# Optimization experiments

Measured on AMD Instinct MI355X. Metric: run time of the kernel, lower is better.

The kernel has to match this reference:

```python
import jax, jax.numpy as jnp
import numpy as np

N = 100_000      # nodes
E = 1_600_000    # edges (avg degree 16)
D_IN = 128
D_OUT = 128
K = 64           # low-rank attention rank


def setup_inputs() -> dict:
    key = jax.random.key(0)
    ks = jax.random.split(key, 6)
    s = lambda d: 1.0 / np.sqrt(d)
    return {
        "x": jax.random.normal(ks[0], (N, D_IN), dtype=jnp.float32),
        "edge_index": jax.random.randint(ks[1], (2, E), 0, N, dtype=jnp.int32),
        "W_gcn": jax.random.normal(ks[2], (D_IN, D_OUT), dtype=jnp.float32) * s(D_IN),
        "b_gcn": jnp.zeros((D_OUT,), jnp.float32),
        "W_att": jax.random.normal(ks[3], (D_IN, 4 * K), dtype=jnp.float32) * s(D_IN),
        "b_att": jnp.zeros((4 * K,), jnp.float32),
        "W_red": jax.random.normal(ks[4], (D_OUT + 2 * K, D_OUT), dtype=jnp.float32) * s(D_OUT + 2 * K),
        "b_red": jnp.zeros((D_OUT,), jnp.float32),
    }


def _forward(x, W_gcn, b_gcn, W_att, b_att, W_red, b_red, edge_index):
    n = x.shape[0]
    # --- GCN conv (symmetric normalization, self-loops), dropout = identity (eval) ---
    loop = jnp.arange(n, dtype=edge_index.dtype)
    src = jnp.concatenate([edge_index[0], loop])
    dst = jnp.concatenate([edge_index[1], loop])
    deg = jax.ops.segment_sum(jnp.ones_like(dst, dtype=x.dtype), dst, num_segments=n)
    dinv = jax.lax.rsqrt(deg)                      # deg >= 1 due to self-loops
    norm = dinv[src] * dinv[dst]                   # [E+n]
    h = x @ W_gcn                                  # [n, D_OUT]
    agg = jax.ops.segment_sum(h[src] * norm[:, None], dst, num_segments=n) + b_gcn
    x_local = jax.nn.relu(agg)

    # --- Low-rank global attention (LRGA) ---
    t = jax.nn.relu(x @ W_att + b_att)             # [n, 4K]
    U, V, Z, T = jnp.split(t, 4, axis=1)           # each [n, K]
    # joint_normalize2: scalar 1/mean(U @ (V^T @ 1_n))
    D = 1.0 / jnp.mean(U @ (V.T @ jnp.ones((n, 1), x.dtype)))
    res = (U @ (V.T @ Z)) * D                      # [n, K]
    x_global = jnp.concatenate([res, T], axis=1)   # [n, 2K]

    # --- fuse + dim reduce ---
    return jnp.concatenate([x_local, x_global], axis=1) @ W_red + b_red


def reference(x, edge_index, W_gcn, b_gcn, W_att, b_att, W_red, b_red):
    return _forward(x, W_gcn, b_gcn, W_att, b_att, W_red, b_red, edge_index)
```

## Files before the change

kernel.cpp:

```cpp
#include <hip/hip_runtime.h>

#define DIN   128
#define DOUT  128
#define KR    64
#define TCOLS 256
#define WCOLS 384
#define P_RED 1024
#define PSTR  4224

typedef unsigned short ushort_t;
typedef __attribute__((ext_vector_type(8))) short bf16x8;
typedef __attribute__((ext_vector_type(4))) float f32x4;

__device__ __forceinline__ float bf2f(unsigned short u) {
  return __uint_as_float(((unsigned int)u) << 16);
}
__device__ __forceinline__ unsigned short f2bf(float f) {
  unsigned int b = __float_as_uint(f);
  b = b + 0x7FFFu + ((b >> 16) & 1u);
  return (unsigned short)(b >> 16);
}

__global__ __launch_bounds__(256) void k_init(int* __restrict__ degc, float* __restrict__ VtZ,
                                              float* __restrict__ colsum, int N) {
  int i = blockIdx.x * 256 + threadIdx.x;
  if (i < N) degc[i] = 1;
  if (i < 4096) VtZ[i] = 0.f;
  if (i < 128) colsum[i] = 0.f;
}

__global__ __launch_bounds__(256) void k_deg(const int* __restrict__ ei, int* __restrict__ degc, int E) {
  int e = blockIdx.x * 256 + threadIdx.x;
  if (e < E) atomicAdd(&degc[ei[E + e]], 1);
}

__global__ __launch_bounds__(256) void k_split(const float* __restrict__ x,
                                               ushort_t* __restrict__ xh, ushort_t* __restrict__ xl4,
                                               int total4) {
  int i = blockIdx.x * 256 + threadIdx.x;
  int stride = gridDim.x * 256;
  for (; i < total4; i += stride) {
    float4 v = ((const float4*)x)[i];
    ushort4 h, l;
    h.x = f2bf(v.x); h.y = f2bf(v.y); h.z = f2bf(v.z); h.w = f2bf(v.w);
    l.x = f2bf(v.x - bf2f(h.x)); l.y = f2bf(v.y - bf2f(h.y));
    l.z = f2bf(v.z - bf2f(h.z)); l.w = f2bf(v.w - bf2f(h.w));
    ((ushort4*)xh)[i] = h;
    ((ushort4*)xl4)[i] = l;
  }
}

__global__ __launch_bounds__(128) void k_wprep(const float* __restrict__ Wg, const float* __restrict__ Wa,
                                               ushort_t* __restrict__ whT, ushort_t* __restrict__ wlT) {
  int n = blockIdx.x;
  int k = threadIdx.x;
  float v = (n < DOUT) ? Wg[(size_t)k * DOUT + n] : Wa[(size_t)k * TCOLS + (n - DOUT)];
  ushort_t h = f2bf(v);
  whT[(size_t)n * DIN + k] = h;
  wlT[(size_t)n * DIN + k] = f2bf(v - bf2f(h));
}

__global__ __launch_bounds__(256) void k_scan1(const int* __restrict__ degc, int* __restrict__ offs,
                                               int* __restrict__ bsums, int N) {
  __shared__ int s[256];
  int tid = threadIdx.x;
  int base = blockIdx.x * 1024 + tid * 4;
  int c[4], e[4];
#pragma unroll
  for (int q = 0; q < 4; ++q) c[q] = (base + q < N) ? (degc[base + q] - 1) : 0;
  e[0] = 0; e[1] = c[0]; e[2] = e[1] + c[1]; e[3] = e[2] + c[2];
  int tsum = e[3] + c[3];
  s[tid] = tsum; __syncthreads();
  for (int off = 1; off < 256; off <<= 1) {
    int v = (tid >= off) ? s[tid - off] : 0;
    __syncthreads();
    s[tid] += v;
    __syncthreads();
  }
  int tb = s[tid] - tsum;
#pragma unroll
  for (int q = 0; q < 4; ++q) if (base + q < N) offs[base + q] = tb + e[q];
  if (tid == 255) bsums[blockIdx.x] = s[255];
}

__global__ __launch_bounds__(128) void k_scan2(const int* __restrict__ bsums, int* __restrict__ boff,
                                               int* __restrict__ offs, int NBLK, int N) {
  __shared__ int s[128];
  int tid = threadIdx.x;
  int v = (tid < NBLK) ? bsums[tid] : 0;
  s[tid] = v; __syncthreads();
  for (int off = 1; off < 128; off <<= 1) {
    int u = (tid >= off) ? s[tid - off] : 0;
    __syncthreads();
    s[tid] += u;
    __syncthreads();
  }
  boff[tid] = s[tid] - v;
  if (tid == 127) offs[N] = s[127];
}

__global__ __launch_bounds__(256) void k_scan3(int* __restrict__ offs, const int* __restrict__ boff,
                                               const int* __restrict__ degc, float* __restrict__ dinv,
                                               int* __restrict__ cursor, int N) {
  int i = blockIdx.x * 256 + threadIdx.x;
  if (i < N) {
    offs[i] += boff[i >> 10];
    dinv[i] = rsqrtf((float)degc[i]);
    cursor[i] = 0;
  }
}

__global__ __launch_bounds__(256) void k_scatter(const int* __restrict__ ei, const int* __restrict__ offs,
                                                 int* __restrict__ cursor, const float* __restrict__ dinv,
                                                 int2* __restrict__ csr, int E) {
  int e = blockIdx.x * 256 + threadIdx.x;
  if (e < E) {
    int s = ei[e];
    int d = ei[E + e];
    int pos = atomicAdd(&cursor[d], 1);
    int2 q;
    q.x = s;
    q.y = __float_as_int(dinv[s] * dinv[d]);
    csr[offs[d] + pos] = q;
  }
}

#define LOADK(S, AH, AL, BH, BL)                                              \
  {                                                                           \
    int k0_ = (S) * 32 + lk;                                                  \
    _Pragma("unroll") for (int m_ = 0; m_ < 4; ++m_) {                        \
      AH[m_] = *(const bf16x8*)&xh[(size_t)rows[m_] * DIN + k0_];             \
      AL[m_] = *(const bf16x8*)&xlo[(size_t)rows[m_] * DIN + k0_];            \
    }                                                                         \
    _Pragma("unroll") for (int n_ = 0; n_ < 4; ++n_) {                        \
      int gc_ = gcb + n_ * 16 + lr;                                           \
      BH[n_] = *(const bf16x8*)&whT[(size_t)gc_ * DIN + k0_];                 \
      BL[n_] = *(const bf16x8*)&wlT[(size_t)gc_ * DIN + k0_];                 \
    }                                                                         \
  }

__global__ __launch_bounds__(256, 2) void k_gemm1_mfma(const ushort_t* __restrict__ xh,
                                                       const ushort_t* __restrict__ xlo,
                                                       const ushort_t* __restrict__ whT,
                                                       const ushort_t* __restrict__ wlT,
                                                       const float* __restrict__ ba,
                                                       ushort_t* __restrict__ hs, ushort_t* __restrict__ t,
                                                       int N) {
  int tid = threadIdx.x;
  int lane = tid & 63;
  int wave = tid >> 6;
  int wr = wave >> 1, wc = wave & 1;
  int colblk = blockIdx.x;
  int rowbase = blockIdx.y * 128 + wr * 64;
  int gcb = colblk * 128 + wc * 64;
  int lr = lane & 15;
  int lk = (lane >> 4) * 8;
  int rq = (lane >> 4) * 4;

  int rows[4];
#pragma unroll
  for (int m = 0; m < 4; ++m) {
    int r = rowbase + m * 16 + lr;
    rows[m] = (r < N) ? r : (N - 1);
  }

  f32x4 acc[4][4] = {};
  bf16x8 ah[2][4], al[2][4], bh[2][4], bl[2][4];

  LOADK(0, ah[0], al[0], bh[0], bl[0]);
#pragma unroll
  for (int s = 0; s < 4; ++s) {
    int cur = s & 1, nxt = cur ^ 1;
    if (s < 3) LOADK(s + 1, ah[nxt], al[nxt], bh[nxt], bl[nxt]);
#pragma unroll
    for (int m = 0; m < 4; ++m)
#pragma unroll
      for (int n = 0; n < 4; ++n) {
        acc[m][n] = __builtin_amdgcn_mfma_f32_16x16x32_bf16(ah[cur][m], bl[cur][n], acc[m][n], 0, 0, 0);
        acc[m][n] = __builtin_amdgcn_mfma_f32_16x16x32_bf16(al[cur][m], bh[cur][n], acc[m][n], 0, 0, 0);
        acc[m][n] = __builtin_amdgcn_mfma_f32_16x16x32_bf16(ah[cur][m], bh[cur][n], acc[m][n], 0, 0, 0);
      }
  }

  if (colblk == 0) {
#pragma unroll
    for (int m = 0; m < 4; ++m)
#pragma unroll
      for (int i = 0; i < 4; ++i) {
        int row = rowbase + m * 16 + rq + i;
        if (row < N) {
#pragma unroll
          for (int n = 0; n < 4; ++n)
            hs[(size_t)row * DOUT + gcb + n * 16 + lr] = f2bf(acc[m][n][i]);
        }
      }
  } else {
    float bav[4];
#pragma unroll
    for (int n = 0; n < 4; ++n) bav[n] = ba[gcb - DOUT + n * 16 + lr];
#pragma unroll
    for (int m = 0; m < 4; ++m)
#pragma unroll
      for (int i = 0; i < 4; ++i) {
        int row = rowbase + m * 16 + rq + i;
        if (row < N) {
#pragma unroll
          for (int n = 0; n < 4; ++n)
            t[(size_t)row * TCOLS + gcb - DOUT + n * 16 + lr] =
                f2bf(fmaxf(acc[m][n][i] + bav[n], 0.f));
        }
      }
  }
}

__global__ __launch_bounds__(256) void k_red(const ushort_t* __restrict__ t, float* __restrict__ part,
                                             int N) {
  __shared__ float csh[512];
  int tid = threadIdx.x;
  int lane = tid & 63;
  int w = tid >> 6;
  int lr = lane & 15;
  int lk = (lane >> 4) * 8;
  int vcol = 64 + w * 16 + lr;
  int col2 = lane * 2;

  f32x4 acc[4] = {};
  float cs0 = 0.f, cs1 = 0.f;
  int ntiles = (N + 31) >> 5;

  for (int tile = blockIdx.x; tile < ntiles; tile += gridDim.x) {
    int r0 = tile * 32;
    const ushort_t* base = &t[(size_t)r0 * TCOLS];
    bf16x8 a, b[4];
    if (r0 + 32 <= N) {
#pragma unroll
      for (int j = 0; j < 8; ++j)
        ((short*)&a)[j] = (short)base[(size_t)(lk + j) * TCOLS + vcol];
#pragma unroll
      for (int n = 0; n < 4; ++n)
#pragma unroll
        for (int j = 0; j < 8; ++j)
          ((short*)&b[n])[j] = (short)base[(size_t)(lk + j) * TCOLS + 128 + n * 16 + lr];
#pragma unroll
      for (int j = 0; j < 8; ++j) {
        ushort2 u = *(const ushort2*)&base[(size_t)(w * 8 + j) * TCOLS + col2];
        cs0 += bf2f(u.x); cs1 += bf2f(u.y);
      }
    } else {
#pragma unroll
      for (int j = 0; j < 8; ++j) {
        int r = r0 + lk + j;
        ((short*)&a)[j] = (r < N) ? (short)t[(size_t)r * TCOLS + vcol] : (short)0;
      }
#pragma unroll
      for (int n = 0; n < 4; ++n)
#pragma unroll
        for (int j = 0; j < 8; ++j) {
          int r = r0 + lk + j;
          ((short*)&b[n])[j] = (r < N) ? (short)t[(size_t)r * TCOLS + 128 + n * 16 + lr] : (short)0;
        }
#pragma unroll
      for (int j = 0; j < 8; ++j) {
        int r = r0 + w * 8 + j;
        if (r < N) {
          ushort2 u = *(const ushort2*)&t[(size_t)r * TCOLS + col2];
          cs0 += bf2f(u.x); cs1 += bf2f(u.y);
        }
      }
    }
#pragma unroll
    for (int n = 0; n < 4; ++n)
      acc[n] = __builtin_amdgcn_mfma_f32_16x16x32_bf16(a, b[n], acc[n], 0, 0, 0);
  }

  float* pb = &part[(size_t)blockIdx.x * PSTR];
  int rq = (lane >> 4) * 4;
#pragma unroll
  for (int n = 0; n < 4; ++n)
#pragma unroll
    for (int i = 0; i < 4; ++i)
      pb[(w * 16 + rq + i) * 64 + n * 16 + lr] = acc[n][i];

  csh[tid] = cs0;
  csh[256 + tid] = cs1;
  __syncthreads();
  if (w == 0) {
    float t0 = csh[lane] + csh[64 + lane] + csh[128 + lane] + csh[192 + lane];
    float t1 = csh[256 + lane] + csh[320 + lane] + csh[384 + lane] + csh[448 + lane];
    pb[4096 + col2] = t0;
    pb[4096 + col2 + 1] = t1;
  }
}

__global__ __launch_bounds__(256) void k_redsum(const float* __restrict__ part,
                                                float* __restrict__ VtZ, float* __restrict__ colsum) {
  __shared__ float s[256];
  int tid = threadIdx.x;
  int j = blockIdx.x * 64 + (tid & 63);
  int bc = tid >> 6;
  float a = 0.f;
#pragma unroll 4
  for (int b = bc; b < P_RED; b += 4) a += part[(size_t)b * PSTR + j];
  s[tid] = a;
  __syncthreads();
  if (bc == 0) {
    float v = s[tid] + s[tid + 64] + s[tid + 128] + s[tid + 192];
    if (j < 4096) VtZ[j] = v;
    else colsum[j - 4096] = v;
  }
}

__global__ __launch_bounds__(64) void k_d(const float* __restrict__ colsum, float* __restrict__ Dws, int N) {
  __shared__ float s[64];
  int k = threadIdx.x;
  s[k] = colsum[k] * colsum[64 + k];
  __syncthreads();
  for (int off = 32; off > 0; off >>= 1) {
    if (k < off) s[k] += s[k + off];
    __syncthreads();
  }
  if (k == 0) {
    float p = s[0];
    Dws[0] = (p != 0.f) ? ((float)N / p) : 0.f;
  }
}

__global__ __launch_bounds__(256) void k_prep(const float* __restrict__ VtZ,
                                              const float* __restrict__ Dws,
                                              const float* __restrict__ Wr,
                                              ushort_t* __restrict__ weffT) {
  int c = blockIdx.x;
  int k = threadIdx.x;
  float v;
  if (k < 128 || k >= 192) {
    v = Wr[(size_t)k * DOUT + c];
  } else {
    float Dv = Dws[0];
    int kk = k - 128;
    float acc = 0.f;
#pragma unroll 8
    for (int j = 0; j < 64; ++j)
      acc += VtZ[kk * 64 + j] * Wr[(size_t)(128 + j) * DOUT + c];
    v = acc * Dv;
  }
  weffT[(size_t)c * 256 + k] = f2bf(v);
}

__global__ __launch_bounds__(256) void k_out_mfma(const ushort_t* __restrict__ xl,
                                                  const ushort_t* __restrict__ t,
                                                  const ushort_t* __restrict__ weffT,
                                                  const float* __restrict__ br,
                                                  float* __restrict__ out, int N) {
  int tid = threadIdx.x;
  int lane = tid & 63;
  int wave = tid >> 6;
  int wr = wave >> 1, wc = wave & 1;
  int rowbase = blockIdx.x * 128 + wr * 64;
  int cbase = wc * 64;
  int lr = lane & 15;
  int lk = (lane >> 4) * 8;

  int rows[4];
#pragma unroll
  for (int m = 0; m < 4; ++m) {
    int r = rowbase + m * 16 + lr;
    rows[m] = (r < N) ? r : (N - 1);
  }

  f32x4 acc[4][4] = {};

#pragma unroll
  for (int s = 0; s < 8; ++s) {
    int k0 = s * 32 + lk;
    bf16x8 a[4], b[4];
#pragma unroll
    for (int m = 0; m < 4; ++m) {
      const ushort_t* ap;
      if (s < 4)      ap = &xl[(size_t)rows[m] * DOUT + k0];
      else if (s < 6) ap = &t[(size_t)rows[m] * TCOLS + (k0 - 128)];
      else            ap = &t[(size_t)rows[m] * TCOLS + k0];
      a[m] = *(const bf16x8*)ap;
    }
#pragma unroll
    for (int n = 0; n < 4; ++n) {
      int c = cbase + n * 16 + lr;
      b[n] = *(const bf16x8*)&weffT[(size_t)c * 256 + k0];
    }
#pragma unroll
    for (int m = 0; m < 4; ++m)
#pragma unroll
      for (int n = 0; n < 4; ++n)
        acc[m][n] = __builtin_amdgcn_mfma_f32_16x16x32_bf16(a[m], b[n], acc[m][n], 0, 0, 0);
  }

  float brv[4];
#pragma unroll
  for (int n = 0; n < 4; ++n) brv[n] = br[cbase + n * 16 + lr];

  int rq = (lane >> 4) * 4;
#pragma unroll
  for (int m = 0; m < 4; ++m) {
#pragma unroll
    for (int i = 0; i < 4; ++i) {
      int row = rowbase + m * 16 + rq + i;
      if (row < N) {
#pragma unroll
        for (int n = 0; n < 4; ++n)
          out[(size_t)row * DOUT + cbase + n * 16 + lr] = acc[m][n][i] + brv[n];
      }
    }
  }
}

__global__ __launch_bounds__(256) void k_aggn(const ushort_t* __restrict__ hs, const int2* __restrict__ csr,
                                              const int* __restrict__ offs, const float* __restrict__ dinv,
                                              const float* __restrict__ bg,
                                              ushort_t* __restrict__ xl, int N) {
  int node = blockIdx.x * 4 + (threadIdx.x >> 6);
  int lane = threadIdx.x & 63;
  if (node >= N) return;
  int c2 = 2 * lane;
  float dn = dinv[node];
  ushort2 u = *(const ushort2*)&hs[(size_t)node * DOUT + c2];
  float a0 = dn * dn * bf2f(u.x);
  float a1 = dn * dn * bf2f(u.y);
  int e = offs[node], e1 = offs[node + 1];
  for (; e + 4 <= e1; e += 4) {
    int2 q0 = csr[e], q1 = csr[e + 1], q2 = csr[e + 2], q3 = csr[e + 3];
    ushort2 r0 = *(const ushort2*)&hs[(size_t)q0.x * DOUT + c2];
    ushort2 r1 = *(const ushort2*)&hs[(size_t)q1.x * DOUT + c2];
    ushort2 r2 = *(const ushort2*)&hs[(size_t)q2.x * DOUT + c2];
    ushort2 r3 = *(const ushort2*)&hs[(size_t)q3.x * DOUT + c2];
    float n0 = __int_as_float(q0.y), n1 = __int_as_float(q1.y);
    float n2 = __int_as_float(q2.y), n3 = __int_as_float(q3.y);
    a0 += n0 * bf2f(r0.x) + n1 * bf2f(r1.x) + n2 * bf2f(r2.x) + n3 * bf2f(r3.x);
    a1 += n0 * bf2f(r0.y) + n1 * bf2f(r1.y) + n2 * bf2f(r2.y) + n3 * bf2f(r3.y);
  }
  for (; e < e1; ++e) {
    int2 q = csr[e];
    ushort2 r = *(const ushort2*)&hs[(size_t)q.x * DOUT + c2];
    float n0 = __int_as_float(q.y);
    a0 += n0 * bf2f(r.x);
    a1 += n0 * bf2f(r.y);
  }
  ushort2 o;
  o.x = f2bf(fmaxf(a0 + bg[c2], 0.f));
  o.y = f2bf(fmaxf(a1 + bg[c2 + 1], 0.f));
  *(ushort2*)&xl[(size_t)node * DOUT + c2] = o;
}

extern "C" void kernel_launch(void* const* d_in, const int* in_sizes, int n_in,
                              void* d_out, int out_size, void* d_ws, size_t ws_size,
                              hipStream_t stream) {
  const float* x  = (const float*)d_in[0];
  const int* ei   = (const int*)d_in[1];
  const float* Wg = (const float*)d_in[2];
  const float* bg = (const float*)d_in[3];
  const float* Wa = (const float*)d_in[4];
  const float* ba = (const float*)d_in[5];
  const float* Wr = (const float*)d_in[6];
  const float* br = (const float*)d_in[7];
  float* out = (float*)d_out;

  const int N = in_sizes[0] / DIN;
  const int E = in_sizes[1] / 2;

  char* p = (char*)d_ws;
  auto alloc = [&](size_t bytes) {
    char* r = p;
    p += (bytes + 255) & ~(size_t)255;
    return r;
  };
  float* Dws    = (float*)alloc(256);
  float* colsum = (float*)alloc(128 * 4);
  float* VtZ    = (float*)alloc(4096 * 4);
  int*   bsums  = (int*)alloc(1024);
  int*   boff   = (int*)alloc(1024);
  ushort_t* weffT = (ushort_t*)alloc(128 * 256 * 2);
  ushort_t* whT = (ushort_t*)alloc((size_t)WCOLS * DIN * 2);
  ushort_t* wlT = (ushort_t*)alloc((size_t)WCOLS * DIN * 2);
  float* part   = (float*)alloc((size_t)P_RED * PSTR * 4);
  int*   degc   = (int*)alloc((size_t)N * 4);
  float* dinv   = (float*)alloc((size_t)N * 4);
  int*   offs   = (int*)alloc((size_t)(N + 1) * 4);
  int*   cursor = (int*)alloc((size_t)N * 4);
  int2*  csr    = (int2*)alloc((size_t)E * 8);
  ushort_t* xh  = (ushort_t*)alloc((size_t)N * DIN * 2);
  ushort_t* xlo = (ushort_t*)alloc((size_t)N * DIN * 2);
  ushort_t* hs  = (ushort_t*)alloc((size_t)N * DOUT * 2);
  ushort_t* t   = (ushort_t*)alloc((size_t)N * TCOLS * 2);
  ushort_t* xl  = (ushort_t*)alloc((size_t)N * DOUT * 2);
  (void)ws_size; (void)n_in; (void)out_size;

  const int GN = (N + 255) / 256;
  const int GE = (E + 255) / 256;
  const int NBLK = (N + 1023) / 1024;

  k_init<<<GN, 256, 0, stream>>>(degc, VtZ, colsum, N);
  k_deg<<<GE, 256, 0, stream>>>(ei, degc, E);
  k_split<<<2048, 256, 0, stream>>>(x, xh, xlo, N * DIN / 4);
  k_wprep<<<WCOLS, 128, 0, stream>>>(Wg, Wa, whT, wlT);
  k_scan1<<<NBLK, 256, 0, stream>>>(degc, offs, bsums, N);
  k_scan2<<<1, 128, 0, stream>>>(bsums, boff, offs, NBLK, N);
  k_scan3<<<GN, 256, 0, stream>>>(offs, boff, degc, dinv, cursor, N);
  k_scatter<<<GE, 256, 0, stream>>>(ei, offs, cursor, dinv, csr, E);
  k_gemm1_mfma<<<dim3(3, (N + 127) / 128), 256, 0, stream>>>(xh, xlo, whT, wlT, ba, hs, t, N);
  k_red<<<P_RED, 256, 0, stream>>>(t, part, N);
  k_redsum<<<PSTR / 64, 256, 0, stream>>>(part, VtZ, colsum);
  k_d<<<1, 64, 0, stream>>>(colsum, Dws, N);
  k_prep<<<128, 256, 0, stream>>>(VtZ, Dws, Wr, weffT);
  k_aggn<<<(N + 3) / 4, 256, 0, stream>>>(hs, csr, offs, dinv, bg, xl, N);
  k_out_mfma<<<(N + 127) / 128, 256, 0, stream>>>(xl, t, weffT, br, out, N);
}
```

Measured before the change: 520.3 us.

## Shard CSR scatter by destination range and remap GEMM1 blocks for locality

The edge scatter kernel now uses a grid-stride loop in which each of 8 block groups handles only destinations in its own eighth of the node range. The intent is to keep cursor atomics and CSR writes localized, presumably per XCD via round-robin block placement. The GEMM1 launch becomes a 1D grid with a swizzle that groups 8 row tiles by 3 column blocks, so blocks that share A rows run close together, and it drops the occupancy hint of 2. The cost is that every shard reads the full destination array (8x the reads of ei[E..]), and removing the launch-bounds hint may change register allocation.

```diff
diff --git a/kernel.cpp b/kernel.cpp
--- a/kernel.cpp
+++ b/kernel.cpp
@@ -112,16 +112,22 @@
 
 __global__ __launch_bounds__(256) void k_scatter(const int* __restrict__ ei, const int* __restrict__ offs,
                                                  int* __restrict__ cursor, const float* __restrict__ dinv,
-                                                 int2* __restrict__ csr, int E) {
-  int e = blockIdx.x * 256 + threadIdx.x;
-  if (e < E) {
-    int s = ei[e];
+                                                 int2* __restrict__ csr, int E, int N, int shardN) {
+  int shard = blockIdx.x & 7;
+  int lo = shard * shardN;
+  int hi = min(lo + shardN, N);
+  int e = (blockIdx.x >> 3) * 256 + threadIdx.x;
+  int stride = (gridDim.x >> 3) * 256;
+  for (; e < E; e += stride) {
     int d = ei[E + e];
-    int pos = atomicAdd(&cursor[d], 1);
-    int2 q;
-    q.x = s;
-    q.y = __float_as_int(dinv[s] * dinv[d]);
-    csr[offs[d] + pos] = q;
+    if (d >= lo && d < hi) {
+      int s = ei[e];
+      int pos = atomicAdd(&cursor[d], 1);
+      int2 q;
+      q.x = s;
+      q.y = __float_as_int(dinv[s] * dinv[d]);
+      csr[offs[d] + pos] = q;
+    }
   }
 }
 
@@ -139,19 +145,25 @@
     }                                                                         \
   }
 
-__global__ __launch_bounds__(256, 2) void k_gemm1_mfma(const ushort_t* __restrict__ xh,
-                                                       const ushort_t* __restrict__ xlo,
-                                                       const ushort_t* __restrict__ whT,
-                                                       const ushort_t* __restrict__ wlT,
-                                                       const float* __restrict__ ba,
-                                                       ushort_t* __restrict__ hs, ushort_t* __restrict__ t,
-                                                       int N) {
+__global__ __launch_bounds__(256) void k_gemm1_mfma(const ushort_t* __restrict__ xh,
+                                                    const ushort_t* __restrict__ xlo,
+                                                    const ushort_t* __restrict__ whT,
+                                                    const ushort_t* __restrict__ wlT,
+                                                    const float* __restrict__ ba,
+                                                    ushort_t* __restrict__ hs, ushort_t* __restrict__ t,
+                                                    int N, int ntiles) {
+  int bid = blockIdx.x;
+  int g = bid / 24;
+  int rem = bid - g * 24;
+  int colblk = rem >> 3;
+  int ytile = g * 8 + (rem & 7);
+  if (ytile >= ntiles) return;
+
   int tid = threadIdx.x;
   int lane = tid & 63;
   int wave = tid >> 6;
   int wr = wave >> 1, wc = wave & 1;
-  int colblk = blockIdx.x;
-  int rowbase = blockIdx.y * 128 + wr * 64;
+  int rowbase = ytile * 128 + wr * 64;
   int gcb = colblk * 128 + wc * 64;
   int lr = lane & 15;
   int lk = (lane >> 4) * 8;
@@ -495,6 +507,9 @@
   const int GN = (N + 255) / 256;
   const int GE = (E + 255) / 256;
   const int NBLK = (N + 1023) / 1024;
+  const int NT128 = (N + 127) / 128;
+  const int G1 = ((NT128 + 7) / 8) * 24;
+  const int shardN = (N + 7) / 8;
 
   k_init<<<GN, 256, 0, stream>>>(degc, VtZ, colsum, N);
   k_deg<<<GE, 256, 0, stream>>>(ei, degc, E);
@@ -503,8 +518,8 @@
   k_scan1<<<NBLK, 256, 0, stream>>>(degc, offs, bsums, N);
   k_scan2<<<1, 128, 0, stream>>>(bsums, boff, offs, NBLK, N);
   k_scan3<<<GN, 256, 0, stream>>>(offs, boff, degc, dinv, cursor, N);
-  k_scatter<<<GE, 256, 0, stream>>>(ei, offs, cursor, dinv, csr, E);
-  k_gemm1_mfma<<<dim3(3, (N + 127) / 128), 256, 0, stream>>>(xh, xlo, whT, wlT, ba, hs, t, N);
+  k_scatter<<<2048, 256, 0, stream>>>(ei, offs, cursor, dinv, csr, E, N, shardN);
+  k_gemm1_mfma<<<G1, 256, 0, stream>>>(xh, xlo, whT, wlT, ba, hs, t, N, NT128);
   k_red<<<P_RED, 256, 0, stream>>>(t, part, N);
   k_redsum<<<PSTR / 64, 256, 0, stream>>>(part, VtZ, colsum);
   k_d<<<1, 64, 0, stream>>>(colsum, Dws, N);
```

Result: no change. 523.6 us (+0.6%).
